# Kernel tuning notes

Measured on AMD Instinct MI355X. Metric: run time of the kernel, lower is better.

## Reference

```python
import jax, jax.numpy as jnp
import numpy as np

B, C, H, W = 4, 512, 64, 64
CQ = C // 8


def setup_inputs() -> dict:
    key = jax.random.key(0)
    ks = jax.random.split(key, 8)
    s_in = 1.0 / np.sqrt(C)
    return {
        "x": jax.random.normal(ks[0], (B, C, H, W), jnp.float32),
        "wq": jax.random.normal(ks[1], (CQ, C), jnp.float32) * s_in,
        "bq": jax.random.normal(ks[2], (CQ,), jnp.float32) * 0.01,
        "wk": jax.random.normal(ks[3], (CQ, C), jnp.float32) * s_in,
        "bk": jax.random.normal(ks[4], (CQ,), jnp.float32) * 0.01,
        "wv": jax.random.normal(ks[5], (C, C), jnp.float32) * s_in,
        "bv": jax.random.normal(ks[6], (C,), jnp.float32) * 0.01,
        "gamma": jax.random.normal(ks[7], (1,), jnp.float32) * 0.1,
    }


def reference(x, wq, bq, wk, bk, wv, bv, gamma):
    b, c, h, w = x.shape
    n = h * w
    xf = x.reshape(b, c, n)  # [B, C, N]; 1x1 conv == channel matmul
    q = jnp.einsum("oc,bcn->bon", wq, xf) + bq[None, :, None]  # [B, CQ, N]
    k = jnp.einsum("oc,bcn->bon", wk, xf) + bk[None, :, None]  # [B, CQ, N]
    v = jnp.einsum("oc,bcn->bon", wv, xf) + bv[None, :, None]  # [B, C, N]
    energy = jnp.einsum("bcn,bcm->bnm", q, k)  # [B, N, N]
    attn = jax.nn.softmax(energy, axis=-1)
    out = jnp.einsum("bcm,bnm->bcn", v, attn)  # [B, C, N]
    out = out.reshape(b, c, h, w)
    return gamma[0] * out + x
```

## Files before the change

### kernel.cpp

```cpp
#include <hip/hip_runtime.h>
#include <hip/hip_bf16.h>

#define BATCH 4
#define CH    512
#define NPIX  4096
#define LOG2E 1.4426950408889634f

#define BOFF  327680
#define WTOT  328320
#define PSTR 264

typedef float v4f __attribute__((ext_vector_type(4)));
typedef short v8s __attribute__((ext_vector_type(8)));
typedef unsigned short u16;

__device__ __forceinline__ float b2f(u16 v){
    union { unsigned u; float f; } x; x.u = ((unsigned)v) << 16; return x.f;
}
__device__ __forceinline__ u16 f2b(float f){
    union { float f; unsigned u; } x; x.f = f;
    unsigned r = x.u + 0x7fffu + ((x.u >> 16) & 1u);
    return (u16)(r >> 16);
}
__device__ __forceinline__ void f2b2(float a, float b, u16* o){
    union { __hip_bfloat162 v; u16 s[2]; } u;
    u.v = __float22bfloat162_rn(make_float2(a, b));
    o[0] = u.s[0]; o[1] = u.s[1];
}
__device__ __forceinline__ v4f mfma16(v8s a, v8s b, v4f c){
    return __builtin_amdgcn_mfma_f32_16x16x32_bf16(a, b, c, 0, 0, 0);
}
__device__ __forceinline__ float load_s(const void* p, size_t idx, int isf32){
    return isf32 ? ((const float*)p)[idx] : b2f(((const u16*)p)[idx]);
}

__global__ void detect_kernel(const unsigned* __restrict__ x, int* __restrict__ flag){
    __shared__ int cnt;
    if (threadIdx.x == 0) cnt = 0;
    __syncthreads();
    int c = 0;
    for (int i = threadIdx.x; i < 1024; i += 64){
        unsigned e = (x[i] >> 23) & 0xFFu;
        if (e >= 64u && e < 192u) c++;
    }
    atomicAdd(&cnt, c);
    __syncthreads();
    if (threadIdx.x == 0) flag[0] = (cnt > 512) ? 1 : 0;
}

__global__ __launch_bounds__(256) void prep_kernel(
    const void* __restrict__ wq, const void* __restrict__ bq,
    const void* __restrict__ wk, const void* __restrict__ bk,
    const void* __restrict__ wv, const void* __restrict__ bv,
    u16* __restrict__ wall, const int* __restrict__ flag)
{
    const int isf32 = flag[0];
    int i = blockIdx.x * 256 + threadIdx.x;
    if (i >= WTOT) return;
    float v;
    if (i < BOFF){
        int o = i >> 9, c = i & 511;
        if (o < 64)       v = load_s(wq, (size_t)o * 512 + c, isf32);
        else if (o < 128) v = load_s(wk, (size_t)(o - 64) * 512 + c, isf32);
        else              v = load_s(wv, (size_t)(o - 128) * 512 + c, isf32);
    } else {
        int o = i - BOFF;
        if (o < 64)       v = load_s(bq, o, isf32);
        else if (o < 128) v = load_s(bk, o - 64, isf32);
        else              v = load_s(bv, o - 128, isf32);
    }
    wall[i] = f2b(v);
}

__global__ __launch_bounds__(512, 2) void proj_kernel(
    const void* __restrict__ x, const u16* __restrict__ wall,
    u16* __restrict__ Qf, u16* __restrict__ Kf, u16* __restrict__ Vf,
    u16* __restrict__ xbf, const int* __restrict__ flag)
{
    const int isf32 = flag[0];
    const int ntile = blockIdx.x, b = blockIdx.y;
    const int n0 = ntile * 64;
    const int t = threadIdx.x, lane = t & 63, w = t >> 6, q = lane >> 4, col = lane & 15;

    __shared__ __align__(16) u16 xT[2][64 * 40];

    const int rrow  = t >> 4;
    const int ncol4 = (t & 15) * 4;
    const size_t xbase = (size_t)b * CH * NPIX + n0 + ncol4;

    v4f acc[5][4];
    #pragma unroll
    for (int i = 0; i < 5; i++)
        #pragma unroll
        for (int j = 0; j < 4; j++) acc[i][j] = (v4f){0.f, 0.f, 0.f, 0.f};

    #define LOADX(dst_f4, cb_) do {                                          \
        const size_t src = xbase + (size_t)((cb_) * 32 + rrow) * NPIX;       \
        if (isf32) dst_f4 = *(const float4*)((const float*)x + src);         \
        else {                                                               \
            union { uint2 v; float2 f; } ldu;                                \
            ldu.v = *(const uint2*)((const u16*)x + src);                    \
            dst_f4.x = ldu.f.x; dst_f4.y = ldu.f.y; dst_f4.z = 0; dst_f4.w = 0; \
        }                                                                    \
    } while (0)

    #define CVT4(vals_, f4_) do {                                            \
        if (isf32){ f2b2(f4_.x, f4_.y, &vals_[0]); f2b2(f4_.z, f4_.w, &vals_[2]); } \
        else { union { float2 f; uint2 v; } uu; uu.f = make_float2(f4_.x, f4_.y);   \
               union { uint2 v; u16 s[4]; } ss; ss.v = uu.v;                 \
               vals_[0]=ss.s[0]; vals_[1]=ss.s[1]; vals_[2]=ss.s[2]; vals_[3]=ss.s[3]; } \
    } while (0)

    float4 g_next;
    {
        float4 g0; LOADX(g0, 0);
        u16 vals[4]; CVT4(vals, g0);
        #pragma unroll
        for (int i = 0; i < 4; i++) xT[0][(ncol4 + i) * 40 + rrow] = vals[i];
        *(uint2*)&xbf[(size_t)(b * CH + rrow) * NPIX + n0 + ncol4] = *(uint2*)vals;
        LOADX(g_next, 1);
    }
    __syncthreads();

    for (int cb = 0; cb < 16; cb++){
        const int buf = cb & 1;
        const int c0 = cb * 32 + q * 8;

        v8s wf[5];
        #pragma unroll
        for (int ct = 0; ct < 5; ct++)
            wf[ct] = *(const v8s*)&wall[(size_t)(80 * w + 16 * ct + col) * 512 + c0];

        v8s a[4];
        #pragma unroll
        for (int g = 0; g < 4; g++)
            a[g] = *(const v8s*)&xT[buf][(16 * g + col) * 40 + q * 8];

        if (cb < 15){
            u16 vals[4]; CVT4(vals, g_next);
            #pragma unroll
            for (int i = 0; i < 4; i++) xT[buf ^ 1][(ncol4 + i) * 40 + rrow] = vals[i];
            *(uint2*)&xbf[(size_t)(b * CH + (cb + 1) * 32 + rrow) * NPIX + n0 + ncol4] = *(uint2*)vals;
            if (cb < 14) LOADX(g_next, cb + 2);
        }

        #pragma unroll
        for (int ct = 0; ct < 5; ct++)
            #pragma unroll
            for (int g = 0; g < 4; g++)
                acc[ct][g] = mfma16(a[g], wf[ct], acc[ct][g]);
        __syncthreads();
    }
    #undef LOADX
    #undef CVT4

    const u16* ball = wall + BOFF;
    #pragma unroll
    for (int ct = 0; ct < 5; ct++){
        const int o = 80 * w + 16 * ct + col;
        const float bv_ = b2f(ball[o]);
        #pragma unroll
        for (int g = 0; g < 4; g++){
            const int nb = n0 + 16 * g + 4 * q;
            if (o < 64){
                const int k = o;
                size_t base = (size_t)b * NPIX * 64
                    + ((size_t)((nb >> 4) * 2 + (k >> 5))) * 512
                    + ((k & 31) >> 3) * 128 + (nb & 15) * 8 + (k & 7);
                #pragma unroll
                for (int r = 0; r < 4; r++)
                    Qf[base + r * 8] = f2b((acc[ct][g][r] + bv_) * LOG2E);
            } else if (o < 128){
                const int k = o - 64;
                size_t base = (size_t)b * NPIX * 64
                    + ((size_t)((nb >> 4) * 2 + (k >> 5))) * 512
                    + ((k & 31) >> 3) * 128 + (nb & 15) * 8 + (k & 7);
                #pragma unroll
                for (int r = 0; r < 4; r++)
                    Kf[base + r * 8] = f2b(acc[ct][g][r] + bv_);
            } else {
                const int c = o - 128;
                size_t base = (size_t)b * CH * NPIX
                    + ((size_t)((c >> 4) * 128 + (nb >> 5))) * 512
                    + ((nb & 31) >> 3) * 128 + (c & 15) * 8 + (nb & 7);
                union { uint2 u; u16 s[4]; } ov;
                #pragma unroll
                for (int r = 0; r < 4; r++)
                    ov.s[r] = f2b(acc[ct][g][r] + bv_);
                *(uint2*)&Vf[base] = ov.u;
            }
        }
    }
}

__global__ __launch_bounds__(512, 2) void attn_kernel(
    const u16* __restrict__ Qf, const u16* __restrict__ Kf, const u16* __restrict__ Vf,
    const u16* __restrict__ xbf, const void* __restrict__ gamma,
    void* __restrict__ out, const int* __restrict__ flag)
{
    const int isf32 = flag[0];
    const int bid = blockIdx.x;
    const int csplit = bid & 1;
    const int b      = (bid >> 1) & 3;
    const int ntile  = bid >> 3;
    const int n0 = ntile * 128;

    const int t = threadIdx.x, lane = t & 63, w = t >> 6, q = lane >> 4, col = lane & 15;
    const int nh = w & 1;
    const int ws = w >> 1;

    __shared__ __align__(16) u16  Plds[2][128 * PSTR];
    __shared__ __align__(16) float lsum[8][64];

    const u16* Qb = Qf + (size_t)b * NPIX * 64;
    const u16* Kb = Kf + (size_t)b * NPIX * 64;
    const u16* Vb = Vf + (size_t)b * CH * NPIX;

    v8s qa[4][2];
    #pragma unroll
    for (int g = 0; g < 4; g++)
        #pragma unroll
        for (int c2 = 0; c2 < 2; c2++)
            qa[g][c2] = *(const v8s*)&Qb[(size_t)((((n0 + 64 * nh) >> 4) + g) * 2 + c2) * 512 + lane * 8];

    float lreg[4][4];
    #pragma unroll
    for (int g = 0; g < 4; g++)
        #pragma unroll
        for (int r = 0; r < 4; r++) lreg[g][r] = 0.f;

    v4f oacc[4][4];
    #pragma unroll
    for (int i = 0; i < 4; i++)
        #pragma unroll
        for (int j = 0; j < 4; j++) oacc[i][j] = (v4f){0.f, 0.f, 0.f, 0.f};

    const int ms    = 64 * ws;
    const int cslab = csplit * 256 + 64 * ws;

    for (int it = 0; it < 16; it++){
        const int m0 = it * 256;
        const int buf = it & 1;

        v8s kf[4][2];
        #pragma unroll
        for (int mt = 0; mt < 4; mt++)
            #pragma unroll
            for (int c2 = 0; c2 < 2; c2++)
                kf[mt][c2] = *(const v8s*)&Kb[(size_t)((((m0 + ms) >> 4) + mt) * 2 + c2) * 512 + lane * 8];

        #pragma unroll
        for (int g = 0; g < 4; g++){
            #pragma unroll
            for (int mt = 0; mt < 4; mt++){
                v4f sv = (v4f){-64.f, -64.f, -64.f, -64.f};
                sv = mfma16(qa[g][0], kf[mt][0], sv);
                sv = mfma16(qa[g][1], kf[mt][1], sv);
                #pragma unroll
                for (int r = 0; r < 4; r++){
                    float p = exp2f(fminf(sv[r], 30.f));
                    lreg[g][r] += p;
                    Plds[buf][(64 * nh + 16 * g + 4 * q + r) * PSTR + ms + 16 * mt + col] = f2b(p);
                }
            }
        }

        __syncthreads();

        v8s va_c[4];
        #pragma unroll
        for (int ct = 0; ct < 4; ct++)
            va_c[ct] = *(const v8s*)&Vb[(size_t)(((cslab + 16 * ct) >> 4) * 128 + (m0 >> 5)) * 512 + lane * 8];
        #pragma unroll
        for (int kk = 0; kk < 8; kk++){
            v8s va_n[4];
            if (kk < 7){
                #pragma unroll
                for (int ct = 0; ct < 4; ct++)
                    va_n[ct] = *(const v8s*)&Vb[(size_t)(((cslab + 16 * ct) >> 4) * 128 + (m0 >> 5) + kk + 1) * 512 + lane * 8];
            }
            v8s pb[4];
            #pragma unroll
            for (int nt = 0; nt < 4; nt++)
                pb[nt] = *(const v8s*)&Plds[buf][(64 * nh + 16 * nt + col) * PSTR + 32 * kk + q * 8];
            #pragma unroll
            for (int ct = 0; ct < 4; ct++)
                #pragma unroll
                for (int nt = 0; nt < 4; nt++)
                    oacc[ct][nt] = mfma16(va_c[ct], pb[nt], oacc[ct][nt]);
            #pragma unroll
            for (int ct = 0; ct < 4; ct++) va_c[ct] = va_n[ct];
        }
    }

    #pragma unroll
    for (int mk = 1; mk < 16; mk <<= 1)
        #pragma unroll
        for (int g = 0; g < 4; g++)
            #pragma unroll
            for (int r = 0; r < 4; r++)
                lreg[g][r] += __shfl_xor(lreg[g][r], mk);
    if (col == 0){
        #pragma unroll
        for (int g = 0; g < 4; g++)
            #pragma unroll
            for (int r = 0; r < 4; r++)
                lsum[w][16 * g + 4 * q + r] = lreg[g][r];
    }
    __syncthreads();

    const float gam = load_s(gamma, 0, isf32);
    float linv[4];
    #pragma unroll
    for (int nt = 0; nt < 4; nt++){
        int nn = 16 * nt + col;
        float l = lsum[nh][nn] + lsum[2 + nh][nn] + lsum[4 + nh][nn] + lsum[6 + nh][nn];
        linv[nt] = gam / l;
    }

    const size_t boff = (size_t)b * CH * NPIX;
    #pragma unroll
    for (int ct = 0; ct < 4; ct++){
        #pragma unroll
        for (int rr = 0; rr < 4; rr++){
            int c = cslab + 16 * ct + 4 * q + rr;
            size_t base = boff + (size_t)c * NPIX + n0 + 64 * nh;
            #pragma unroll
            for (int nt = 0; nt < 4; nt++){
                int n = 16 * nt + col;
                float o = oacc[ct][nt][rr] * linv[nt] + b2f(xbf[base + n]);
                if (isf32) ((float*)out)[base + n] = o;
                else       ((u16*)out)[base + n]  = f2b(o);
            }
        }
    }
}

extern "C" void kernel_launch(void* const* d_in, const int* in_sizes, int n_in,
                              void* d_out, int out_size, void* d_ws, size_t ws_size,
                              hipStream_t stream)
{
    const void* x     = d_in[0];
    const void* wq    = d_in[1];
    const void* bq    = d_in[2];
    const void* wk    = d_in[3];
    const void* bk    = d_in[4];
    const void* wv    = d_in[5];
    const void* bv    = d_in[6];
    const void* gamma = d_in[7];

    u16* Qf   = (u16*)d_ws;
    u16* Kf   = Qf + (size_t)1048576;
    u16* Vf   = Kf + (size_t)1048576;
    u16* xbf  = Vf + (size_t)8388608;
    u16* wall = xbf + (size_t)8388608;
    int* flag = (int*)(wall + WTOT + 16);

    detect_kernel<<<1, 64, 0, stream>>>((const unsigned*)x, flag);
    prep_kernel<<<(WTOT + 255) / 256, 256, 0, stream>>>(wq, bq, wk, bk, wv, bv, wall, flag);
    proj_kernel<<<dim3(64, BATCH), 512, 0, stream>>>(x, wall, Qf, Kf, Vf, xbf, flag);
    attn_kernel<<<256, 512, 0, stream>>>(Qf, Kf, Vf, xbf, gamma, d_out, flag);
}
```

Measured before the change: 234.7 us.

## Retile projection kernel and transpose score MFMA for packed P stores

The projection kernel now handles 32 pixels per block instead of 64 and walks channels in chunks of 64. That doubles the grid and allows higher occupancy through launch_bounds. The attention kernel swaps the MFMA operands so each lane holds four consecutive keys of one query row, which lets it write P to LDS as one packed 8-byte store and cuts the row-sum reduction to two shuffles. It also drops the clamp before exp2, uses the hardware exp2 builtin, and changes the P row padding. Removing the clamp risks overflow if scores ever exceed the offset, and re-reading the weights more often adds global traffic.

```diff
diff --git a/kernel.cpp b/kernel.cpp
--- a/kernel.cpp
+++ b/kernel.cpp
@@ -8,7 +8,7 @@
 
 #define BOFF  327680
 #define WTOT  328320
-#define PSTR 264
+#define PSTR  268
 
 typedef float v4f __attribute__((ext_vector_type(4)));
 typedef short v8s __attribute__((ext_vector_type(8)));
@@ -26,6 +26,13 @@
     union { __hip_bfloat162 v; u16 s[2]; } u;
     u.v = __float22bfloat162_rn(make_float2(a, b));
     o[0] = u.s[0]; o[1] = u.s[1];
+}
+__device__ __forceinline__ float fexp2(float x){
+#if __has_builtin(__builtin_amdgcn_exp2f)
+    return __builtin_amdgcn_exp2f(x);
+#else
+    return exp2f(x);
+#endif
 }
 __device__ __forceinline__ v4f mfma16(v8s a, v8s b, v4f c){
     return __builtin_amdgcn_mfma_f32_16x16x32_bf16(a, b, c, 0, 0, 0);
@@ -72,30 +79,30 @@
     wall[i] = f2b(v);
 }
 
-__global__ __launch_bounds__(512, 2) void proj_kernel(
+__global__ __launch_bounds__(512, 4) void proj_kernel(
     const void* __restrict__ x, const u16* __restrict__ wall,
     u16* __restrict__ Qf, u16* __restrict__ Kf, u16* __restrict__ Vf,
     u16* __restrict__ xbf, const int* __restrict__ flag)
 {
     const int isf32 = flag[0];
-    const int ntile = blockIdx.x, b = blockIdx.y;
-    const int n0 = ntile * 64;
+    const int nt2 = blockIdx.x, b = blockIdx.y;
+    const int n0 = nt2 * 32;
     const int t = threadIdx.x, lane = t & 63, w = t >> 6, q = lane >> 4, col = lane & 15;
 
-    __shared__ __align__(16) u16 xT[2][64 * 40];
-
-    const int rrow  = t >> 4;
-    const int ncol4 = (t & 15) * 4;
+    __shared__ __align__(16) u16 xT[2][32 * 72];
+
+    const int rrow  = t >> 3;
+    const int ncol4 = (t & 7) * 4;
     const size_t xbase = (size_t)b * CH * NPIX + n0 + ncol4;
 
-    v4f acc[5][4];
+    v4f acc[5][2];
     #pragma unroll
     for (int i = 0; i < 5; i++)
         #pragma unroll
-        for (int j = 0; j < 4; j++) acc[i][j] = (v4f){0.f, 0.f, 0.f, 0.f};
+        for (int j = 0; j < 2; j++) acc[i][j] = (v4f){0.f, 0.f, 0.f, 0.f};
 
     #define LOADX(dst_f4, cb_) do {                                          \
-        const size_t src = xbase + (size_t)((cb_) * 32 + rrow) * NPIX;       \
+        const size_t src = xbase + (size_t)((cb_) * 64 + rrow) * NPIX;       \
         if (isf32) dst_f4 = *(const float4*)((const float*)x + src);         \
         else {                                                               \
             union { uint2 v; float2 f; } ldu;                                \
@@ -116,39 +123,40 @@
         float4 g0; LOADX(g0, 0);
         u16 vals[4]; CVT4(vals, g0);
         #pragma unroll
-        for (int i = 0; i < 4; i++) xT[0][(ncol4 + i) * 40 + rrow] = vals[i];
+        for (int i = 0; i < 4; i++) xT[0][(ncol4 + i) * 72 + rrow] = vals[i];
         *(uint2*)&xbf[(size_t)(b * CH + rrow) * NPIX + n0 + ncol4] = *(uint2*)vals;
         LOADX(g_next, 1);
     }
     __syncthreads();
 
-    for (int cb = 0; cb < 16; cb++){
+    for (int cb = 0; cb < 8; cb++){
         const int buf = cb & 1;
-        const int c0 = cb * 32 + q * 8;
-
-        v8s wf[5];
-        #pragma unroll
-        for (int ct = 0; ct < 5; ct++)
-            wf[ct] = *(const v8s*)&wall[(size_t)(80 * w + 16 * ct + col) * 512 + c0];
-
-        v8s a[4];
-        #pragma unroll
-        for (int g = 0; g < 4; g++)
-            a[g] = *(const v8s*)&xT[buf][(16 * g + col) * 40 + q * 8];
-
-        if (cb < 15){
+
+        if (cb < 7){
             u16 vals[4]; CVT4(vals, g_next);
             #pragma unroll
-            for (int i = 0; i < 4; i++) xT[buf ^ 1][(ncol4 + i) * 40 + rrow] = vals[i];
-            *(uint2*)&xbf[(size_t)(b * CH + (cb + 1) * 32 + rrow) * NPIX + n0 + ncol4] = *(uint2*)vals;
-            if (cb < 14) LOADX(g_next, cb + 2);
-        }
-
-        #pragma unroll
-        for (int ct = 0; ct < 5; ct++)
-            #pragma unroll
-            for (int g = 0; g < 4; g++)
-                acc[ct][g] = mfma16(a[g], wf[ct], acc[ct][g]);
+            for (int i = 0; i < 4; i++) xT[buf ^ 1][(ncol4 + i) * 72 + rrow] = vals[i];
+            *(uint2*)&xbf[(size_t)(b * CH + (cb + 1) * 64 + rrow) * NPIX + n0 + ncol4] = *(uint2*)vals;
+            if (cb < 6) LOADX(g_next, cb + 2);
+        }
+
+        #pragma unroll
+        for (int kh = 0; kh < 2; kh++){
+            const int c0 = cb * 64 + kh * 32 + q * 8;
+            v8s wf[5];
+            #pragma unroll
+            for (int ct = 0; ct < 5; ct++)
+                wf[ct] = *(const v8s*)&wall[(size_t)(80 * w + 16 * ct + col) * 512 + c0];
+            v8s a[2];
+            #pragma unroll
+            for (int g = 0; g < 2; g++)
+                a[g] = *(const v8s*)&xT[buf][(16 * g + col) * 72 + kh * 32 + q * 8];
+            #pragma unroll
+            for (int ct = 0; ct < 5; ct++)
+                #pragma unroll
+                for (int g = 0; g < 2; g++)
+                    acc[ct][g] = mfma16(a[g], wf[ct], acc[ct][g]);
+        }
         __syncthreads();
     }
     #undef LOADX
@@ -160,7 +168,7 @@
         const int o = 80 * w + 16 * ct + col;
         const float bv_ = b2f(ball[o]);
         #pragma unroll
-        for (int g = 0; g < 4; g++){
+        for (int g = 0; g < 2; g++){
             const int nb = n0 + 16 * g + 4 * q;
             if (o < 64){
                 const int k = o;
@@ -223,11 +231,7 @@
         for (int c2 = 0; c2 < 2; c2++)
             qa[g][c2] = *(const v8s*)&Qb[(size_t)((((n0 + 64 * nh) >> 4) + g) * 2 + c2) * 512 + lane * 8];
 
-    float lreg[4][4];
-    #pragma unroll
-    for (int g = 0; g < 4; g++)
-        #pragma unroll
-        for (int r = 0; r < 4; r++) lreg[g][r] = 0.f;
+    float lreg[4] = {0.f, 0.f, 0.f, 0.f};
 
     v4f oacc[4][4];
     #pragma unroll
@@ -254,14 +258,15 @@
             #pragma unroll
             for (int mt = 0; mt < 4; mt++){
                 v4f sv = (v4f){-64.f, -64.f, -64.f, -64.f};
-                sv = mfma16(qa[g][0], kf[mt][0], sv);
-                sv = mfma16(qa[g][1], kf[mt][1], sv);
-                #pragma unroll
-                for (int r = 0; r < 4; r++){
-                    float p = exp2f(fminf(sv[r], 30.f));
-                    lreg[g][r] += p;
-                    Plds[buf][(64 * nh + 16 * g + 4 * q + r) * PSTR + ms + 16 * mt + col] = f2b(p);
-                }
+                sv = mfma16(kf[mt][0], qa[g][0], sv);
+                sv = mfma16(kf[mt][1], qa[g][1], sv);
+                float p0 = fexp2(sv[0]), p1 = fexp2(sv[1]);
+                float p2 = fexp2(sv[2]), p3 = fexp2(sv[3]);
+                lreg[g] += (p0 + p1) + (p2 + p3);
+                union { uint2 u; u16 s[4]; } pk;
+                f2b2(p0, p1, &pk.s[0]);
+                f2b2(p2, p3, &pk.s[2]);
+                *(uint2*)&Plds[buf][(64 * nh + 16 * g + col) * PSTR + ms + 16 * mt + 4 * q] = pk.u;
             }
         }
 
@@ -294,18 +299,14 @@
     }
 
     #pragma unroll
-    for (int mk = 1; mk < 16; mk <<= 1)
+    for (int g = 0; g < 4; g++){
+        lreg[g] += __shfl_xor(lreg[g], 16);
+        lreg[g] += __shfl_xor(lreg[g], 32);
+    }
+    if (lane < 16){
         #pragma unroll
         for (int g = 0; g < 4; g++)
-            #pragma unroll
-            for (int r = 0; r < 4; r++)
-                lreg[g][r] += __shfl_xor(lreg[g][r], mk);
-    if (col == 0){
-        #pragma unroll
-        for (int g = 0; g < 4; g++)
-            #pragma unroll
-            for (int r = 0; r < 4; r++)
-                lsum[w][16 * g + 4 * q + r] = lreg[g][r];
+            lsum[w][16 * g + lane] = lreg[g];
     }
     __syncthreads();
 
@@ -358,6 +359,6 @@
 
     detect_kernel<<<1, 64, 0, stream>>>((const unsigned*)x, flag);
     prep_kernel<<<(WTOT + 255) / 256, 256, 0, stream>>>(wq, bq, wk, bk, wv, bv, wall, flag);
-    proj_kernel<<<dim3(64, BATCH), 512, 0, stream>>>(x, wall, Qf, Kf, Vf, xbf, flag);
+    proj_kernel<<<dim3(128, BATCH), 512, 0, stream>>>(x, wall, Qf, Kf, Vf, xbf, flag);
     attn_kernel<<<256, 512, 0, stream>>>(Qf, Kf, Vf, xbf, gamma, d_out, flag);
 }
```

After: 254.8 us. +8.6%, slower.
